# Kernel optimization log

Hardware: AMD Instinct MI355X
Metric: run time of the kernel (lower is better)

The kernel has to match this reference:

```python
import jax, jax.numpy as jnp
import numpy as np

B = 512; LH = 200; N = 40000; F = 256; E = 2000000; EF = 4
K = 8; LP = 50; P = 5000; D = 64; TD = 16; SK = 1000


def _time_enc(t):
    # TimeDualDecayEncoder stand-in: fixed log-spaced frequency cosine features (TGAT-style)
    freqs = 1.0 / (10.0 ** (jnp.arange(TD, dtype=jnp.float32) / TD * 5.0))
    return jnp.cos(t[..., None] * freqs)


def _layernorm(x, g, b):
    m = x.mean(-1, keepdims=True)
    v = ((x - m) ** 2).mean(-1, keepdims=True)
    return (x - m) * jax.lax.rsqrt(v + 1e-5) * g + b


def _gru(x, Wih, Whh, bih, bhh):
    # torch nn.GRU (batch_first), gate order r,z,n; returns final hidden state
    bsz, H = x.shape[0], Whh.shape[1]
    def step(h, xt):
        gi = xt @ Wih.T + bih
        gh = h @ Whh.T + bhh
        ir, iz, inn = jnp.split(gi, 3, -1)
        hr, hz, hn = jnp.split(gh, 3, -1)
        r = jax.nn.sigmoid(ir + hr)
        z = jax.nn.sigmoid(iz + hz)
        n = jnp.tanh(inn + r * hn)
        return (1.0 - z) * n + z * h, None
    h, _ = jax.lax.scan(step, jnp.zeros((bsz, H), x.dtype), jnp.swapaxes(x, 0, 1))
    return h


def _forward(src_node_ids, dst_node_ids, local_neighbor_ids, local_edge_ids, local_times,
             dst_neighbor_ids, dst_edge_ids, dst_times, retrieved_indices,
             node_raw, edge_raw, pool_nodes,
             Wfeat, bfeat, Wedge, bedge, Wtime, btime, Wstruct, bstruct, ln_g, ln_b,
             gruL_Wih, gruL_Whh, gruL_bih, gruL_bhh, gruQ_Wih, gruQ_Whh, gruQ_bih, gruQ_bhh,
             gcn_W, gcn_b, fus_W, fus_b, out_W, out_b):

    def dygkt(nids, eids, times, cur_dst, cur_skill):
        raw = node_raw[nids]                                   # (B,L,F) gather
        nf = raw @ Wfeat.T + bfeat
        ef = edge_raw[eids, 0:1] @ Wedge.T + bedge
        tf = _time_enc(times) @ Wtime.T + btime
        co = (nids == cur_dst[:, None]).astype(jnp.float32)[..., None]
        st = co @ Wstruct.T + bstruct
        sim = (raw[..., 0].astype(jnp.int32) == cur_skill[:, None]).astype(jnp.float32)[..., None]
        sk = sim @ Wstruct.T + bstruct
        return _layernorm(nf + ef + tf + st + sk, ln_g, ln_b)

    def graph_emb(demo):
        # demo: (K,LP) padded node-id sequences (0 = pad). Build dedup'd undirected
        # consecutive-pair graph, run GCNConv (self loops, sym norm), mean-pool.
        ids = demo.reshape(-1)
        M = ids.shape[0]
        valid = ids > 0
        sids = jnp.sort(jnp.where(valid, ids, N))               # invalid -> sentinel N
        uniq = (sids < N) & jnp.concatenate([jnp.ones((1,), bool), sids[1:] != sids[:-1]])
        x = node_raw[jnp.clip(sids, 0, N - 1)] @ Wfeat.T + bfeat
        h = (x @ gcn_W.T) * uniq[:, None]
        u = demo[:, :-1].reshape(-1)
        v = demo[:, 1:].reshape(-1)
        ve = (u > 0) & (v > 0)
        a = jnp.minimum(u, v); b = jnp.maximum(u, v)
        BIG = N * N                                             # fits int32 since N=40000
        skey = jnp.sort(jnp.where(ve, a * N + b, BIG))
        ew = ((skey < BIG) & jnp.concatenate([jnp.ones((1,), bool), skey[1:] != skey[:-1]])).astype(x.dtype)
        su = jnp.clip(jnp.searchsorted(sids, skey // N), 0, M - 1)
        sv = jnp.clip(jnp.searchsorted(sids, skey % N), 0, M - 1)
        uf = uniq.astype(x.dtype)
        deg = jnp.zeros(M, x.dtype).at[su].add(ew).at[sv].add(ew) + uf   # + self loop
        dis = jnp.where(deg > 0, jax.lax.rsqrt(deg), 0.0)
        nrm = (ew * dis[su] * dis[sv])[:, None]
        agg = jnp.zeros_like(h).at[sv].add(nrm * h[su]).at[su].add(nrm * h[sv])
        agg = agg + h * (dis * dis)[:, None] + gcn_b * uf[:, None]
        out = jax.nn.relu(agg)
        return out.sum(0) / jnp.maximum(uniq.sum(), 1).astype(x.dtype)

    dst_skill = node_raw[dst_node_ids, 0].astype(jnp.int32)
    src_skill = node_raw[src_node_ids, 0].astype(jnp.int32)
    local_emb = _gru(dygkt(local_neighbor_ids, local_edge_ids, local_times, dst_node_ids, dst_skill),
                     gruL_Wih, gruL_Whh, gruL_bih, gruL_bhh)
    glob = jax.vmap(graph_emb)(pool_nodes[retrieved_indices])   # (B,D)
    q_emb = _gru(dygkt(dst_neighbor_ids, dst_edge_ids, dst_times, src_node_ids, src_skill),
                 gruQ_Wih, gruQ_Whh, gruQ_bih, gruQ_bhh)
    fused = jax.nn.relu(jnp.concatenate([local_emb, glob], 1) @ fus_W.T + fus_b)
    return fused @ out_W.T + out_b, q_emb @ out_W.T + out_b


def setup_inputs() -> dict:
    key = jax.random.key(0)
    ks = jax.random.split(key, 32)
    f32 = jnp.float32
    node_raw = jax.random.normal(ks[0], (N, F), f32)
    node_raw = node_raw.at[:, 0].set(jax.random.randint(ks[1], (N,), 0, SK).astype(f32))
    edge_raw = jax.random.normal(ks[2], (E, EF), f32)
    ids = jax.random.randint(ks[3], (P, LP), 1, N)
    lens = jax.random.randint(ks[4], (P,), 2, LP + 1)
    pool_nodes = jnp.where(jnp.arange(LP)[None, :] < lens[:, None], ids, 0).astype(jnp.int32)
    def lin(k, o, i, s=0.05):
        kw, kb = jax.random.split(k)
        return jax.random.normal(kw, (o, i), f32) * s, jax.random.normal(kb, (o,), f32) * s
    Wfeat, bfeat = lin(ks[5], D, F)
    Wedge, bedge = lin(ks[6], D, 1)
    Wtime, btime = lin(ks[7], D, TD)
    Wstruct, bstruct = lin(ks[8], D, 1)
    gruL_Wih, gruL_bih = lin(ks[9], 3 * D, D)
    gruL_Whh, gruL_bhh = lin(ks[10], 3 * D, D)
    gruQ_Wih, gruQ_bih = lin(ks[11], 3 * D, D)
    gruQ_Whh, gruQ_bhh = lin(ks[12], 3 * D, D)
    gcn_W, gcn_b = lin(ks[13], D, D)
    fus_W, fus_b = lin(ks[14], D, 2 * D)
    out_W, out_b = lin(ks[15], D, D)
    return dict(
        src_node_ids=jax.random.randint(ks[16], (B,), 0, N).astype(jnp.int32),
        dst_node_ids=jax.random.randint(ks[17], (B,), 0, N).astype(jnp.int32),
        local_neighbor_ids=jax.random.randint(ks[18], (B, LH), 0, N).astype(jnp.int32),
        local_edge_ids=jax.random.randint(ks[19], (B, LH), 0, E).astype(jnp.int32),
        local_times=jax.random.uniform(ks[20], (B, LH), f32) * 100.0,
        dst_neighbor_ids=jax.random.randint(ks[21], (B, LH), 0, N).astype(jnp.int32),
        dst_edge_ids=jax.random.randint(ks[22], (B, LH), 0, E).astype(jnp.int32),
        dst_times=jax.random.uniform(ks[23], (B, LH), f32) * 100.0,
        retrieved_indices=jax.random.randint(ks[24], (B, K), 0, P).astype(jnp.int32),
        node_raw=node_raw, edge_raw=edge_raw, pool_nodes=pool_nodes,
        Wfeat=Wfeat, bfeat=bfeat, Wedge=Wedge, bedge=bedge, Wtime=Wtime, btime=btime,
        Wstruct=Wstruct, bstruct=bstruct, ln_g=jnp.ones((D,), f32), ln_b=jnp.zeros((D,), f32),
        gruL_Wih=gruL_Wih, gruL_Whh=gruL_Whh, gruL_bih=gruL_bih, gruL_bhh=gruL_bhh,
        gruQ_Wih=gruQ_Wih, gruQ_Whh=gruQ_Whh, gruQ_bih=gruQ_bih, gruQ_bhh=gruQ_bhh,
        gcn_W=gcn_W, gcn_b=gcn_b, fus_W=fus_W, fus_b=fus_b, out_W=out_W, out_b=out_b)


def reference(src_node_ids, dst_node_ids, local_neighbor_ids, local_edge_ids, local_times,
              dst_neighbor_ids, dst_edge_ids, dst_times, retrieved_indices,
              node_raw, edge_raw, pool_nodes,
              Wfeat, bfeat, Wedge, bedge, Wtime, btime, Wstruct, bstruct, ln_g, ln_b,
              gruL_Wih, gruL_Whh, gruL_bih, gruL_bhh, gruQ_Wih, gruQ_Whh, gruQ_bih, gruQ_bhh,
              gcn_W, gcn_b, fus_W, fus_b, out_W, out_b):
    return _forward(src_node_ids, dst_node_ids, local_neighbor_ids, local_edge_ids, local_times,
                    dst_neighbor_ids, dst_edge_ids, dst_times, retrieved_indices,
                    node_raw, edge_raw, pool_nodes,
                    Wfeat, bfeat, Wedge, bedge, Wtime, btime, Wstruct, bstruct, ln_g, ln_b,
                    gruL_Wih, gruL_Whh, gruL_bih, gruL_bhh, gruQ_Wih, gruQ_Whh, gruQ_bih, gruQ_bhh,
                    gcn_W, gcn_b, fus_W, fus_b, out_W, out_b)
```

## Files before the change

### kernel.cpp

```cpp
#include <hip/hip_runtime.h>
#include <math.h>

#define NN 40000
#define FF 256
#define DD 64
#define LHH 200
#define BB 512
#define TDD 16
#define GE_HASH 1024

typedef _Float16 h2f __attribute__((ext_vector_type(2)));

__constant__ float TFREQ[16] = {
    1.0f,            0.48696753f,    0.23713737f,    0.115478195f,
    0.056234132f,    0.027384196f,   0.013335215f,   0.0064938162f,
    0.0031622776f,   0.0015399265f,  0.00074989421f, 0.00036517414f,
    0.00017782794f,  8.6596433e-05f, 4.2169650e-05f, 2.0535251e-05f
};

__device__ __forceinline__ float fd2(unsigned a, unsigned b, float c) {
    union { unsigned u; h2f h; } ua, ub;
    ua.u = a; ub.u = b;
    return __builtin_amdgcn_fdot2(ua.h, ub.h, c, false);
}
__device__ __forceinline__ unsigned packrn(float a, float b) {
    union { h2f h; unsigned u; } x;
    x.h.x = (_Float16)a; x.h.y = (_Float16)b;
    return x.u;
}
__device__ __forceinline__ unsigned short f16u(float a) {
    union { _Float16 h; unsigned short u; } x;
    x.h = (_Float16)a;
    return x.u;
}
__device__ __forceinline__ float h16f(unsigned short u) {
    union { unsigned short u; _Float16 h; } x;
    x.u = u;
    return (float)x.h;
}
__device__ __forceinline__ float f16lo(unsigned u) {
    union { unsigned u; h2f h; } x; x.u = u; return (float)x.h.x;
}
__device__ __forceinline__ float f16hi(unsigned u) {
    union { unsigned u; h2f h; } x; x.u = u; return (float)x.h.y;
}
__device__ __forceinline__ unsigned pkrtz_u(float a, float b) {
    auto pk = __builtin_amdgcn_cvt_pkrtz(a, b);
    union { decltype(pk) h; unsigned u; } x;
    x.h = pk;
    return x.u;
}
__device__ __forceinline__ float dpp_xor1(float v) {
    return __int_as_float(
        __builtin_amdgcn_mov_dpp(__float_as_int(v), 0xB1, 0xF, 0xF, true));
}
__device__ __forceinline__ unsigned rlu(unsigned v, int l) {
    return (unsigned)__builtin_amdgcn_readlane((int)v, l);
}
__device__ __forceinline__ float sigm(float x) {
    return __builtin_amdgcn_rcpf(1.f + __expf(-x));
}
__device__ __forceinline__ float tanh_f(float x) {
    float e = __expf(2.f * x);
    return 1.f - 2.f * __builtin_amdgcn_rcpf(e + 1.f);
}
__device__ __forceinline__ int hlookupf(const unsigned* hkey, const int* hslot, unsigned id)
{
    unsigned p = (id * 2654435761u) & (GE_HASH - 1);
    while (hkey[p] != id) p = (p + 1) & (GE_HASH - 1);
    return hslot[p];
}

__global__ void __launch_bounds__(256)
compact_kernel(const float* __restrict__ node_raw, unsigned short* __restrict__ skill16)
{
    int i = blockIdx.x * 256 + threadIdx.x;
    if (i < NN) skill16[i] = (unsigned short)(int)node_raw[(size_t)i * FF];
}

template<int KDIM>
__global__ void __launch_bounds__(256)
gemm_nt_kernel(const float* __restrict__ A, const float* __restrict__ W,
               const float* __restrict__ bias, float* __restrict__ C, int Nrows)
{
    __shared__ __align__(16) float a_t[128][8];
    __shared__ __align__(16) float wt[8][64];
    const int tid = threadIdx.x;
    const int tx = tid & 15;
    const int ty = tid >> 4;
    const int n0 = blockIdx.x * 128;

    float4 acc[8];
#pragma unroll
    for (int r = 0; r < 8; ++r) acc[r] = make_float4(0.f, 0.f, 0.f, 0.f);

    for (int kc = 0; kc < KDIM; kc += 8) {
        __syncthreads();
        {
            int r = tid >> 1;
            int cc = (tid & 1) * 4;
            int n = n0 + r;
            float4 v = make_float4(0.f, 0.f, 0.f, 0.f);
            if (n < Nrows) v = *(const float4*)(A + (size_t)n * KDIM + kc + cc);
            *(float4*)&a_t[r][cc] = v;
        }
        {
            int m = tid >> 2;
            int f0 = (tid & 3) * 2;
            float2 v = *(const float2*)(W + (size_t)m * KDIM + kc + f0);
            wt[f0][m] = v.x; wt[f0 + 1][m] = v.y;
        }
        __syncthreads();
        float4 w4[8];
#pragma unroll
        for (int f = 0; f < 8; ++f) w4[f] = *(float4*)&wt[f][tx * 4];
#pragma unroll
        for (int rr = 0; rr < 8; ++rr) {
            int row = ty + rr * 16;
            float4 a0 = *(float4*)&a_t[row][0];
            float4 a1 = *(float4*)&a_t[row][4];
            float av[8] = {a0.x, a0.y, a0.z, a0.w, a1.x, a1.y, a1.z, a1.w};
#pragma unroll
            for (int f = 0; f < 8; ++f) {
                acc[rr].x += av[f] * w4[f].x;
                acc[rr].y += av[f] * w4[f].y;
                acc[rr].z += av[f] * w4[f].z;
                acc[rr].w += av[f] * w4[f].w;
            }
        }
    }
    float4 bv = make_float4(0.f, 0.f, 0.f, 0.f);
    if (bias) bv = *(const float4*)(bias + tx * 4);
#pragma unroll
    for (int rr = 0; rr < 8; ++rr) {
        int n = n0 + ty + rr * 16;
        if (n < Nrows) {
            float4 o = acc[rr];
            o.x += bv.x; o.y += bv.y; o.z += bv.z; o.w += bv.w;
            *(float4*)(C + (size_t)n * DD + tx * 4) = o;
        }
    }
}

__global__ void __launch_bounds__(256)
tn_gemm_kernel(const float* __restrict__ proj,
               const float* __restrict__ WihL, const float* __restrict__ WihQ,
               const float* __restrict__ ln_g,
               unsigned short* __restrict__ Tn4L, unsigned short* __restrict__ Tn4Q)
{
    const float* Wih = blockIdx.y ? WihQ : WihL;
    unsigned short* Tn4 = blockIdx.y ? Tn4Q : Tn4L;
    __shared__ float wgT[64][193];
    __shared__ __align__(16) float4 at4[64][16];
    const int tid = threadIdx.x;
    const int n0 = blockIdx.x * 64;
    for (int i = tid; i < 192 * 64; i += 256) {
        int j = i >> 6, k = i & 63;
        wgT[k][j] = Wih[i] * ln_g[k];
    }
    for (int i = tid; i < 1024; i += 256) {
        int r = i >> 4, kc = i & 15;
        at4[r][kc] = ((const float4*)(proj + (size_t)(n0 + r) * DD))[kc];
    }
    __syncthreads();
    const float* atf = (const float*)at4;
    const int c = tid & 63, wv = tid >> 6;
    float acc0[16], acc1[16], acc2[16];
#pragma unroll
    for (int r = 0; r < 16; ++r) { acc0[r] = 0.f; acc1[r] = 0.f; acc2[r] = 0.f; }
    for (int kc = 0; kc < 16; ++kc) {
        float w0[4], w1[4], w2[4];
#pragma unroll
        for (int q = 0; q < 4; ++q) {
            w0[q] = wgT[kc * 4 + q][c];
            w1[q] = wgT[kc * 4 + q][64 + c];
            w2[q] = wgT[kc * 4 + q][128 + c];
        }
#pragma unroll
        for (int r = 0; r < 16; ++r) {
            float4 a = at4[wv * 16 + r][kc];
            acc0[r] += a.x * w0[0] + a.y * w0[1] + a.z * w0[2] + a.w * w0[3];
            acc1[r] += a.x * w1[0] + a.y * w1[1] + a.z * w1[2] + a.w * w1[3];
            acc2[r] += a.x * w2[0] + a.y * w2[1] + a.z * w2[2] + a.w * w2[3];
        }
    }
#pragma unroll
    for (int r = 0; r < 16; ++r) {
        int row = wv * 16 + r;
        unsigned lo = packrn(acc0[r], acc1[r]);
        unsigned hi = packrn(acc2[r], atf[row * 64 + c]);
        uint2 o = make_uint2(lo, hi);
        *(uint2*)(Tn4 + ((size_t)(n0 + row) * 64 + c) * 4) = o;
    }
}

__global__ void __launch_bounds__(192)
consts_kernel(const float* __restrict__ WihL, const float* __restrict__ bihL,
              const float* __restrict__ WhhL, float* __restrict__ outL,
              unsigned* __restrict__ whpL, unsigned* __restrict__ tpkL,
              const float* __restrict__ WihQ, const float* __restrict__ bihQ,
              const float* __restrict__ WhhQ, float* __restrict__ outQ,
              unsigned* __restrict__ whpQ, unsigned* __restrict__ tpkQ,
              unsigned* __restrict__ wtpk,
              const float* __restrict__ ln_g, const float* __restrict__ ln_b,
              const float* __restrict__ Wedge, const float* __restrict__ bedge,
              const float* __restrict__ Wtime, const float* __restrict__ btime,
              const float* __restrict__ Wstruct, const float* __restrict__ bstruct)
{
    const float* Wih = blockIdx.x ? WihQ : WihL;
    const float* bih = blockIdx.x ? bihQ : bihL;
    const float* Whh = blockIdx.x ? WhhQ : WhhL;
    float* out = blockIdx.x ? outQ : outL;
    unsigned* whp = blockIdx.x ? whpQ : whpL;
    unsigned* tpk = blockIdx.x ? tpkQ : tpkL;
    const int j = threadIdx.x;
    float te = 0.f, tw = 0.f, t1 = 0.f, tb0 = 0.f, cc = 0.f;
    float tt[16];
#pragma unroll
    for (int t = 0; t < 16; ++t) tt[t] = 0.f;
    for (int k = 0; k < DD; ++k) {
        float wv = Wih[j * DD + k];
        float wg = wv * ln_g[k];
        te  += wg * Wedge[k];
        tw  += wg * Wstruct[k];
        t1  += wg;
        tb0 += wg * (bedge[k] + btime[k] + 2.f * bstruct[k]);
        cc  += wv * ln_b[k];
#pragma unroll
        for (int t = 0; t < 16; ++t) tt[t] += wg * Wtime[k * TDD + t];
    }
    out[0 * 192 + j] = te;
    out[1 * 192 + j] = tw;
    out[2 * 192 + j] = t1;
    out[3 * 192 + j] = tb0;
    out[4 * 192 + j] = cc + bih[j];
    for (int t = 0; t < 16; ++t) out[(5 + t) * 192 + j] = tt[t];
    for (int q = 0; q < 8; ++q)
        tpk[j * 8 + q] = packrn(tt[2 * q], tt[2 * q + 1]);
    if (blockIdx.x == 0 && j < 64)
        for (int q = 0; q < 8; ++q)
            wtpk[j * 8 + q] = packrn(Wtime[j * TDD + 2 * q], Wtime[j * TDD + 2 * q + 1]);
    for (int k2 = 0; k2 < 32; ++k2)
        whp[j * 32 + k2] = packrn(Whh[j * DD + 2 * k2], Whh[j * DD + 2 * k2 + 1]);
}

struct PS {
    int nid, skI;
    float tn0, tn1, tn2, pv, e0, t;
};

__global__ void __launch_bounds__(256)
pre_kernel(const int* __restrict__ nidsL, const int* __restrict__ eidsL,
           const float* __restrict__ timesL, const int* __restrict__ curL,
           const int* __restrict__ nidsQ, const int* __restrict__ eidsQ,
           const float* __restrict__ timesQ, const int* __restrict__ curQ,
           const unsigned short* __restrict__ skill16, const float* __restrict__ edge_raw,
           const unsigned short* __restrict__ Tn4L, const unsigned short* __restrict__ Tn4Q,
           const float* __restrict__ cstL, const float* __restrict__ cstQ,
           const unsigned* __restrict__ tpkL, const unsigned* __restrict__ tpkQ,
           const unsigned* __restrict__ wtpk,
           const float* __restrict__ bhhL, const float* __restrict__ bhhQ,
           const float* __restrict__ Wedge, const float* __restrict__ bedge,
           const float* __restrict__ Wtime, const float* __restrict__ btime,
           const float* __restrict__ Wstruct, const float* __restrict__ bstruct,
           unsigned* __restrict__ g01out, unsigned short* __restrict__ g2out)
{
    const int tid = threadIdx.x;
    const int d = tid & 63;
    const int seg = blockIdx.x * 4 + (tid >> 6);
    const int blk = seg >> 3, qq = seg & 7;
    const int g = blk >> 9, s = blk & 511;

    const int*            nids  = g ? nidsQ : nidsL;
    const int*            eids  = g ? eidsQ : eidsL;
    const float*          times = g ? timesQ : timesL;
    const int*            curp  = g ? curQ : curL;
    const unsigned short* Tn4   = g ? Tn4Q : Tn4L;
    const float*          cst   = g ? cstQ : cstL;
    const unsigned*       tpk   = g ? tpkQ : tpkL;
    const float*          bhh   = g ? bhhQ : bhhL;

    unsigned tp0[8], tp1[8], tp2[8], wtp[8];
#pragma unroll
    for (int q4 = 0; q4 < 2; ++q4) {
        uint4 a = *(const uint4*)(tpk + (size_t)(0 * 64 + d) * 8 + 4 * q4);
        tp0[4*q4] = a.x; tp0[4*q4+1] = a.y; tp0[4*q4+2] = a.z; tp0[4*q4+3] = a.w;
        uint4 b = *(const uint4*)(tpk + (size_t)(1 * 64 + d) * 8 + 4 * q4);
        tp1[4*q4] = b.x; tp1[4*q4+1] = b.y; tp1[4*q4+2] = b.z; tp1[4*q4+3] = b.w;
        uint4 c = *(const uint4*)(tpk + (size_t)(2 * 64 + d) * 8 + 4 * q4);
        tp2[4*q4] = c.x; tp2[4*q4+1] = c.y; tp2[4*q4+2] = c.z; tp2[4*q4+3] = c.w;
        uint4 e = *(const uint4*)(wtpk + (size_t)d * 8 + 4 * q4);
        wtp[4*q4] = e.x; wtp[4*q4+1] = e.y; wtp[4*q4+2] = e.z; wtp[4*q4+3] = e.w;
    }
    const float TE0 = cst[0*192 + d], TE1 = cst[0*192 + 64 + d], TE2 = cst[0*192 + 128 + d];
    const float TW0 = cst[1*192 + d], TW1 = cst[1*192 + 64 + d], TW2 = cst[1*192 + 128 + d];
    const float T10 = cst[2*192 + d], T11 = cst[2*192 + 64 + d], T12 = cst[2*192 + 128 + d];
    const float TB0 = cst[3*192 + d], TB1 = cst[3*192 + 64 + d], TB2 = cst[3*192 + 128 + d];
    const float CC0 = cst[4*192 + d] + bhh[d];
    const float CC1 = cst[4*192 + 64 + d] + bhh[64 + d];
    const float CC2 = cst[4*192 + 128 + d];
    const float we_l = Wedge[d];
    const float ws_l = Wstruct[d];
    const float b0_l = bedge[d] + btime[d] + 2.f * bstruct[d];
    const float tfl  = TFREQ[d & 15];

    const int cur = curp[s];
    const int csk = (int)skill16[cur];
    const int* nrow = nids + s * LHH;
    const int* erow = eids + s * LHH;
    const float* trow = times + s * LHH;
    const int lbase = qq * 25;

    auto GATH = [&](PS& P, int i) {
        int l = lbase + i;
        int nid = nrow[l];
        int eid = erow[l];
        P.nid = nid;
        uint2 v = *(const uint2*)(Tn4 + ((size_t)nid * 64 + d) * 4);
        P.tn0 = f16lo(v.x);
        P.tn1 = f16hi(v.x);
        P.tn2 = f16lo(v.y);
        P.pv  = f16hi(v.y);
        P.e0  = edge_raw[(size_t)eid * 4];
        P.skI = (int)skill16[nid];
        P.t   = trow[l];
    };

    auto EMIT = [&](const PS& P, int i) {
        float cv = __cosf(P.t * tfl);
        float cx = dpp_xor1(cv);
        unsigned cp = pkrtz_u(cv, cx);
        unsigned s0 = rlu(cp, 0),  s1 = rlu(cp, 2),  s2 = rlu(cp, 4),  s3 = rlu(cp, 6);
        unsigned s4 = rlu(cp, 8),  s5 = rlu(cp, 10), s6 = rlu(cp, 12), s7 = rlu(cp, 14);
        float tf = fd2(wtp[7], s7, fd2(wtp[6], s6, fd2(wtp[5], s5, fd2(wtp[4], s4, 0.f))));
        tf = fd2(wtp[3], s3, fd2(wtp[2], s2, fd2(wtp[1], s1, fd2(wtp[0], s0, tf))));
        float flg = ((P.nid == cur) ? 1.f : 0.f) + ((P.skI == csk) ? 1.f : 0.f);
        float f = P.pv + P.e0 * we_l + flg * ws_l + b0_l + tf;
        float mu = f;
#pragma unroll
        for (int off = 32; off; off >>= 1) mu += __shfl_xor(mu, off);
        mu *= (1.f / 64.f);
        float dv = f - mu, var = dv * dv;
#pragma unroll
        for (int off = 32; off; off >>= 1) var += __shfl_xor(var, off);
        float rs = rsqrtf(var * (1.f / 64.f) + 1e-5f);
        float c0 = fd2(tp0[7], s7, fd2(tp0[6], s6, fd2(tp0[5], s5, fd2(tp0[4], s4, 0.f))));
        c0 = fd2(tp0[3], s3, fd2(tp0[2], s2, fd2(tp0[1], s1, fd2(tp0[0], s0, c0))));
        float c1 = fd2(tp1[7], s7, fd2(tp1[6], s6, fd2(tp1[5], s5, fd2(tp1[4], s4, 0.f))));
        c1 = fd2(tp1[3], s3, fd2(tp1[2], s2, fd2(tp1[1], s1, fd2(tp1[0], s0, c1))));
        float c2 = fd2(tp2[7], s7, fd2(tp2[6], s6, fd2(tp2[5], s5, fd2(tp2[4], s4, 0.f))));
        c2 = fd2(tp2[3], s3, fd2(tp2[2], s2, fd2(tp2[1], s1, fd2(tp2[0], s0, c2))));
        float g0 = (c0 + P.tn0 + P.e0 * TE0 + flg * TW0 + TB0 - mu * T10) * rs + CC0;
        float g1 = (c1 + P.tn1 + P.e0 * TE1 + flg * TW1 + TB1 - mu * T11) * rs + CC1;
        float g2 = (c2 + P.tn2 + P.e0 * TE2 + flg * TW2 + TB2 - mu * T12) * rs + CC2;
        size_t pos = ((size_t)blk * LHH + (lbase + i)) * 64 + d;
        g01out[pos] = packrn(g0, g1);
        g2out[pos] = f16u(g2);
    };

    PS A, B, C;
    GATH(A, 0);
    GATH(B, 1);
    for (int i = 0; i < 25; ++i) {
        int inext = (i + 2 < 25) ? i + 2 : 24;
        GATH(C, inext);
        EMIT(A, i);
        A = B; B = C;
    }
}

__global__ void __launch_bounds__(64) __attribute__((amdgpu_waves_per_eu(1, 1)))
gru_lite_kernel(const unsigned* __restrict__ g01, const unsigned short* __restrict__ g2a,
                const unsigned* __restrict__ whpL, const unsigned* __restrict__ whpQ,
                const float* __restrict__ bhhL, const float* __restrict__ bhhQ,
                float* __restrict__ embL, float* __restrict__ embQ)
{
    const int blk = blockIdx.x;
    const int g = blk >> 9, s = blk & 511;
    const int d = threadIdx.x;

    const unsigned* whp = g ? whpQ : whpL;
    const float*    bhh = g ? bhhQ : bhhL;
    float*          emb = g ? embQ : embL;

    unsigned w0[32], w1[32], w2[32];
    {
        const unsigned* p0 = whp + (size_t)d * 32;
        const unsigned* p1 = whp + (size_t)(64 + d) * 32;
        const unsigned* p2 = whp + (size_t)(128 + d) * 32;
#pragma unroll
        for (int q4 = 0; q4 < 8; ++q4) {
            uint4 a = *(const uint4*)(p0 + 4 * q4);
            w0[4*q4] = a.x; w0[4*q4+1] = a.y; w0[4*q4+2] = a.z; w0[4*q4+3] = a.w;
            uint4 b = *(const uint4*)(p1 + 4 * q4);
            w1[4*q4] = b.x; w1[4*q4+1] = b.y; w1[4*q4+2] = b.z; w1[4*q4+3] = b.w;
            uint4 c = *(const uint4*)(p2 + 4 * q4);
            w2[4*q4] = c.x; w2[4*q4+1] = c.y; w2[4*q4+2] = c.z; w2[4*q4+3] = c.w;
        }
    }
#pragma unroll
    for (int i = 0; i < 32; ++i) {
        asm volatile("" : "+v"(w0[i]));
        asm volatile("" : "+v"(w1[i]));
        asm volatile("" : "+v"(w2[i]));
    }
    const float BH2 = bhh[128 + d];

    const unsigned* p01 = g01 + (size_t)blk * LHH * 64 + d;
    const unsigned short* p2 = g2a + (size_t)blk * LHH * 64 + d;

    float h = 0.f;

    auto COMPUTE = [&](unsigned pk01, unsigned pk2) {
        float g0 = f16lo(pk01), g1 = f16hi(pk01);
        float g2 = h16f((unsigned short)pk2);
        float hx = dpp_xor1(h);
        unsigned hpu = pkrtz_u(h, hx);
        float a0 = 0.f, a1 = 0.f, a2 = 0.f, e0 = 0.f, e1 = 0.f, e2 = 0.f;
#pragma unroll
        for (int q = 0; q < 32; q += 2) {
            unsigned sa = rlu(hpu, 2 * q);
            unsigned sb = rlu(hpu, 2 * q + 2);
            a0 = fd2(w0[q], sa, a0);
            a1 = fd2(w1[q], sa, a1);
            a2 = fd2(w2[q], sa, a2);
            e0 = fd2(w0[q+1], sb, e0);
            e1 = fd2(w1[q+1], sb, e1);
            e2 = fd2(w2[q+1], sb, e2);
        }
        float mv0 = a0 + e0, mv1 = a1 + e1, mv2 = a2 + e2;
        float r = sigm(g0 + mv0);
        float z = sigm(g1 + mv1);
        float n = tanh_f(g2 + r * (mv2 + BH2));
        h = (1.f - z) * n + z * h;
    };

    unsigned A01[4], A2[4], B01[4], B2[4];
#pragma unroll
    for (int i = 0; i < 4; ++i) {
        A01[i] = p01[(size_t)i * 64];
        A2[i]  = p2[(size_t)i * 64];
    }
    for (int l = 0; l < LHH; l += 8) {
#pragma unroll
        for (int i = 0; i < 4; ++i) {
            int ll = l + 4 + i;
            B01[i] = p01[(size_t)ll * 64];
            B2[i]  = p2[(size_t)ll * 64];
        }
#pragma unroll
        for (int i = 0; i < 4; ++i) COMPUTE(A01[i], A2[i]);
#pragma unroll
        for (int i = 0; i < 4; ++i) {
            int ll = l + 8 + i;
            if (ll > LHH - 1) ll = LHH - 1;
            A01[i] = p01[(size_t)ll * 64];
            A2[i]  = p2[(size_t)ll * 64];
        }
#pragma unroll
        for (int i = 0; i < 4; ++i) COMPUTE(B01[i], B2[i]);
    }
    emb[(size_t)s * DD + d] = h;
}

__global__ void __launch_bounds__(512)
dedup_kernel(const int* __restrict__ retrieved, const int* __restrict__ pool_nodes,
             int* __restrict__ slot_idG, float* __restrict__ disG,
             unsigned* __restrict__ startG, unsigned short* __restrict__ adjG,
             int* __restrict__ Ub)
{
    __shared__ unsigned hkey[GE_HASH];
    __shared__ int hslot[GE_HASH];
    __shared__ unsigned ekey[GE_HASH];
    __shared__ int ids[400];
    __shared__ int slot_id[400];
    __shared__ unsigned deg[400];
    __shared__ float dis[400];
    __shared__ unsigned elist[400];
    __shared__ unsigned scanA[400], scanB[400];
    __shared__ int cursor[400];
    __shared__ unsigned short adjS[800];
    __shared__ int pids[8];
    __shared__ int cntU, cntE;

    const int b = blockIdx.x;
    const int tid = threadIdx.x;

    if (tid < 8) pids[tid] = retrieved[b * 8 + tid];
    if (tid == 0) { cntU = 0; cntE = 0; }
    for (int i = tid; i < GE_HASH; i += 512) { hkey[i] = 0u; ekey[i] = 0u; }
    if (tid < 400) deg[tid] = 0u;
    __syncthreads();

    if (tid < 400) {
        int k = tid / 50, p = tid % 50;
        ids[tid] = pool_nodes[(size_t)pids[k] * 50 + p];
    }
    __syncthreads();

    if (tid < 400) {
        int idi = ids[tid];
        if (idi > 0) {
            unsigned id = (unsigned)idi;
            unsigned p = (id * 2654435761u) & (GE_HASH - 1);
            while (true) {
                unsigned old = atomicCAS(&hkey[p], 0u, id);
                if (old == 0u) {
                    int s = atomicAdd(&cntU, 1);
                    hslot[p] = s; slot_id[s] = idi;
                    break;
                }
                if (old == id) break;
                p = (p + 1) & (GE_HASH - 1);
            }
        }
    }
    __syncthreads();

    if (tid < 8 * 49) {
        int k = tid / 49, p = tid % 49;
        int u = ids[k * 50 + p], v = ids[k * 50 + p + 1];
        if (u > 0 && v > 0) {
            unsigned a = (unsigned)min(u, v), bb = (unsigned)max(u, v);
            unsigned key = a * 40000u + bb;
            unsigned p2 = (key * 2654435761u) & (GE_HASH - 1);
            while (true) {
                unsigned old = atomicCAS(&ekey[p2], 0u, key);
                if (old == 0u) {
                    int su = hlookupf(hkey, hslot, a);
                    int sv = hlookupf(hkey, hslot, bb);
                    int e = atomicAdd(&cntE, 1);
                    elist[e] = ((unsigned)su << 16) | (unsigned)sv;
                    atomicAdd(&deg[su], 1u);
                    atomicAdd(&deg[sv], 1u);
                    break;
                }
                if (old == key) break;
                p2 = (p2 + 1) & (GE_HASH - 1);
            }
        }
    }
    __syncthreads();

    const int U = cntU, EC = cntE;
    if (tid < 400) {
        dis[tid] = rsqrtf((float)deg[tid] + 1.0f);
        scanA[tid] = deg[tid];
    }
    __syncthreads();

    unsigned* src = scanA;
    unsigned* dst = scanB;
    for (int off = 1; off < 400; off <<= 1) {
        if (tid < 400)
            dst[tid] = src[tid] + ((tid >= off) ? src[tid - off] : 0u);
        __syncthreads();
        unsigned* t = src; src = dst; dst = t;
    }
    if (tid < 400) {
        unsigned st = src[tid] - deg[tid];
        cursor[tid] = (int)st;
        if (tid < U) startG[(size_t)b * 404 + tid] = st;
    }
    if (tid == 0) {
        startG[(size_t)b * 404 + U] = (U > 0) ? src[U - 1] : 0u;
        Ub[b] = U;
    }
    __syncthreads();

    if (tid < EC) {
        unsigned pk = elist[tid];
        int su = (int)(pk >> 16), sv = (int)(pk & 0xffffu);
        int pu = atomicAdd(&cursor[su], 1);
        adjS[pu] = (unsigned short)sv;
        int pv = atomicAdd(&cursor[sv], 1);
        adjS[pv] = (unsigned short)su;
    }
    __syncthreads();

    if (tid < 400) {
        slot_idG[(size_t)b * 400 + tid] = (tid < U) ? slot_id[tid] : 0;
        disG[(size_t)b * 400 + tid] = dis[tid];
    }
    for (int i = tid; i < 800; i += 512) {
        unsigned tot = (U > 0) ? src[U - 1] : 0u;
        adjG[(size_t)b * 800 + i] = (i < (int)tot) ? adjS[i] : (unsigned short)0;
    }
}

__global__ void __launch_bounds__(256)
gcn_agg_kernel(const float* __restrict__ hgcn, const float* __restrict__ gcn_b,
               const int* __restrict__ slot_idG, const float* __restrict__ disG,
               const unsigned* __restrict__ startG, const unsigned short* __restrict__ adjG,
               const int* __restrict__ Ub, float* __restrict__ part)
{
    __shared__ int sidS[400];
    __shared__ float disS[400];
    __shared__ unsigned stS[404];
    __shared__ unsigned short adjS[800];
    __shared__ float red[4][64];

    const int b = blockIdx.x, q = blockIdx.y;
    const int tid = threadIdx.x;
    const int lane = tid & 63, w = tid >> 6;
    const int U = Ub[b];

    for (int i = tid; i < 400; i += 256) {
        sidS[i] = slot_idG[(size_t)b * 400 + i];
        disS[i] = disG[(size_t)b * 400 + i];
    }
    for (int i = tid; i < 404; i += 256) stS[i] = startG[(size_t)b * 404 + i];
    for (int i = tid; i < 800; i += 256) adjS[i] = adjG[(size_t)b * 800 + i];
    __syncthreads();

    const float gb = gcn_b[lane];
    float acc = 0.f;

    for (int s = q * 4 + w; s < U; s += 16) {
        int nid = sidS[s];
        float ds = disS[s];
        float v = fmaf(ds * ds, hgcn[(size_t)nid * 64 + lane], gb);
        int a0 = (int)stS[s];
        int cnt = (int)stS[s + 1] - a0;
        for (int e0 = 0; e0 < cnt; e0 += 4) {
            float hv[4], nr[4];
#pragma unroll
            for (int j = 0; j < 4; ++j) {
                int e = e0 + j;
                int ec = (e < cnt) ? e : cnt - 1;
                int o = adjS[a0 + ec];
                nr[j] = (e < cnt) ? ds * disS[o] : 0.f;
                hv[j] = hgcn[(size_t)sidS[o] * 64 + lane];
            }
            v += nr[0] * hv[0] + nr[1] * hv[1] + nr[2] * hv[2] + nr[3] * hv[3];
        }
        acc += fmaxf(v, 0.f);
    }

    red[w][lane] = acc;
    __syncthreads();
    if (tid < 64)
        part[((size_t)b * 4 + q) * 64 + tid] =
            red[0][tid] + red[1][tid] + red[2][tid] + red[3][tid];
}

__global__ void __launch_bounds__(64)
head_kernel(const float* __restrict__ local_emb, const float* __restrict__ part,
            const int* __restrict__ Ub, const float* __restrict__ q_emb,
            const float* __restrict__ fus_W, const float* __restrict__ fus_b,
            const float* __restrict__ out_W, const float* __restrict__ out_b,
            float* __restrict__ out)
{
    __shared__ float cat[128];
    __shared__ float fus[64];
    __shared__ float qv[64];
    const int b = blockIdx.x, d = threadIdx.x;
    cat[d] = local_emb[(size_t)b * 64 + d];
    {
        const float* pb = part + (size_t)b * 4 * 64;
        float gsum = pb[d] + pb[64 + d] + pb[128 + d] + pb[192 + d];
        cat[64 + d] = gsum / (float)max(Ub[b], 1);
    }
    qv[d] = q_emb[(size_t)b * 64 + d];
    __syncthreads();
    float acc = fus_b[d];
    const float* fw = fus_W + (size_t)d * 128;
#pragma unroll 4
    for (int k = 0; k < 128; ++k) acc += cat[k] * fw[k];
    fus[d] = fmaxf(acc, 0.f);
    __syncthreads();
    float o0 = out_b[d], o1 = out_b[d];
    const float* ow = out_W + (size_t)d * 64;
#pragma unroll 4
    for (int k = 0; k < 64; ++k) { float ww = ow[k]; o0 += fus[k] * ww; o1 += qv[k] * ww; }
    out[(size_t)b * 64 + d] = o0;
    out[(size_t)BB * 64 + (size_t)b * 64 + d] = o1;
}

extern "C" void kernel_launch(void* const* d_in, const int* in_sizes, int n_in,
                              void* d_out, int out_size, void* d_ws, size_t ws_size,
                              hipStream_t stream)
{
    const int*   src_ids    = (const int*)d_in[0];
    const int*   dst_ids    = (const int*)d_in[1];
    const int*   l_nids     = (const int*)d_in[2];
    const int*   l_eids     = (const int*)d_in[3];
    const float* l_times    = (const float*)d_in[4];
    const int*   d_nids     = (const int*)d_in[5];
    const int*   d_eids     = (const int*)d_in[6];
    const float* d_times    = (const float*)d_in[7];
    const int*   retr       = (const int*)d_in[8];
    const float* node_raw   = (const float*)d_in[9];
    const float* edge_raw   = (const float*)d_in[10];
    const int*   pool_nodes = (const int*)d_in[11];
    const float* Wfeat  = (const float*)d_in[12];
    const float* bfeat  = (const float*)d_in[13];
    const float* Wedge  = (const float*)d_in[14];
    const float* bedge  = (const float*)d_in[15];
    const float* Wtime  = (const float*)d_in[16];
    const float* btime  = (const float*)d_in[17];
    const float* Wstruct= (const float*)d_in[18];
    const float* bstruct= (const float*)d_in[19];
    const float* ln_g   = (const float*)d_in[20];
    const float* ln_b   = (const float*)d_in[21];
    const float* gruL_Wih = (const float*)d_in[22];
    const float* gruL_Whh = (const float*)d_in[23];
    const float* gruL_bih = (const float*)d_in[24];
    const float* gruL_bhh = (const float*)d_in[25];
    const float* gruQ_Wih = (const float*)d_in[26];
    const float* gruQ_Whh = (const float*)d_in[27];
    const float* gruQ_bih = (const float*)d_in[28];
    const float* gruQ_bhh = (const float*)d_in[29];
    const float* gcn_W  = (const float*)d_in[30];
    const float* gcn_b  = (const float*)d_in[31];
    const float* fus_W  = (const float*)d_in[32];
    const float* fus_b  = (const float*)d_in[33];
    const float* out_W  = (const float*)d_in[34];
    const float* out_b  = (const float*)d_in[35];

    char* wsb = (char*)d_ws;
    auto alloc = [&](size_t bytes) -> void* {
        void* p = (void*)wsb;
        wsb += (bytes + 255) & ~(size_t)255;
        return p;
    };
    float*          proj_node = (float*)alloc((size_t)NN * DD * 4);
    float*          hgcn      = (float*)alloc((size_t)NN * DD * 4);
    unsigned short* Tn4L      = (unsigned short*)alloc((size_t)NN * 64 * 4 * 2);
    unsigned short* Tn4Q      = (unsigned short*)alloc((size_t)NN * 64 * 4 * 2);
    unsigned short* skill16   = (unsigned short*)alloc((size_t)NN * 2);
    float*          cstL      = (float*)alloc(4096 * 4);
    float*          cstQ      = (float*)alloc(4096 * 4);
    unsigned*       whpL      = (unsigned*)alloc(192 * 32 * 4);
    unsigned*       whpQ      = (unsigned*)alloc(192 * 32 * 4);
    unsigned*       tpkL      = (unsigned*)alloc(192 * 8 * 4);
    unsigned*       tpkQ      = (unsigned*)alloc(192 * 8 * 4);
    unsigned*       wtpk      = (unsigned*)alloc(64 * 8 * 4);
    unsigned*       g01       = (unsigned*)alloc((size_t)2 * BB * LHH * 64 * 4);
    unsigned short* g2a       = (unsigned short*)alloc((size_t)2 * BB * LHH * 64 * 2);
    int*            slot_idG  = (int*)alloc((size_t)BB * 400 * 4);
    float*          disG      = (float*)alloc((size_t)BB * 400 * 4);
    unsigned*       startG    = (unsigned*)alloc((size_t)BB * 404 * 4);
    unsigned short* adjG      = (unsigned short*)alloc((size_t)BB * 800 * 2);
    int*            Ubuf      = (int*)alloc((size_t)BB * 4);
    float*          part      = (float*)alloc((size_t)BB * 4 * 64 * 4);
    float*          local_emb = (float*)alloc((size_t)BB * DD * 4);
    float*          q_emb     = (float*)alloc((size_t)BB * DD * 4);

    dim3 g1((NN + 127) / 128);
    gemm_nt_kernel<FF><<<g1, 256, 0, stream>>>(node_raw, Wfeat, bfeat, proj_node, NN);

    compact_kernel<<<(NN + 255) / 256, 256, 0, stream>>>(node_raw, skill16);

    consts_kernel<<<2, 192, 0, stream>>>(gruL_Wih, gruL_bih, gruL_Whh, cstL, whpL, tpkL,
                                         gruQ_Wih, gruQ_bih, gruQ_Whh, cstQ, whpQ, tpkQ,
                                         wtpk, ln_g, ln_b, Wedge, bedge, Wtime, btime,
                                         Wstruct, bstruct);

    gemm_nt_kernel<DD><<<g1, 256, 0, stream>>>(proj_node, gcn_W, nullptr, hgcn, NN);

    tn_gemm_kernel<<<dim3(NN / 64, 2), 256, 0, stream>>>(proj_node, gruL_Wih, gruQ_Wih,
                                                         ln_g, Tn4L, Tn4Q);

    dedup_kernel<<<BB, 512, 0, stream>>>(retr, pool_nodes, slot_idG, disG,
                                         startG, adjG, Ubuf);

    pre_kernel<<<2 * BB * 2, 256, 0, stream>>>(
        l_nids, l_eids, l_times, dst_ids,
        d_nids, d_eids, d_times, src_ids,
        skill16, edge_raw, Tn4L, Tn4Q, cstL, cstQ,
        tpkL, tpkQ, wtpk, gruL_bhh, gruQ_bhh,
        Wedge, bedge, Wtime, btime, Wstruct, bstruct,
        g01, g2a);

    gcn_agg_kernel<<<dim3(BB, 4), 256, 0, stream>>>(
        hgcn, gcn_b, slot_idG, disG, startG, adjG, Ubuf, part);

    gru_lite_kernel<<<2 * BB, 64, 0, stream>>>(
        g01, g2a, whpL, whpQ, gruL_bhh, gruQ_bhh, local_emb, q_emb);

    head_kernel<<<BB, 64, 0, stream>>>(local_emb, part, Ubuf, q_emb,
        fus_W, fus_b, out_W, out_b, (float*)d_out);
}
```

Measured before the change: 292.9 us.

## Precompute LayerNorm mean algebraically to remove one wave reduction per row

The LayerNorm mean in pre_kernel is now computed analytically from precomputed per-node row sums of the projected features plus summed weight constants, so only the variance needs a cross-lane reduction. compact_kernel now also writes each node's projected-feature sum packed with its skill id into an 8-byte record, and consts_kernel emits the weight-sum constants. The remaining variance reduction uses DPP row operations instead of a full shuffle chain. This adds a pass over proj_node and slightly larger per-neighbor gathers, and the time-encoding part of the mean is computed with fp16 dot products, which may shift rounding.

Result: no change. 295.2 us (+0.8%).

```diff
diff --git a/kernel.cpp b/kernel.cpp
--- a/kernel.cpp
+++ b/kernel.cpp
@@ -54,6 +54,21 @@
     return __int_as_float(
         __builtin_amdgcn_mov_dpp(__float_as_int(v), 0xB1, 0xF, 0xF, true));
 }
+template<int CTRL>
+__device__ __forceinline__ float dppadd(float v) {
+    float t = __int_as_float(
+        __builtin_amdgcn_mov_dpp(__float_as_int(v), CTRL, 0xF, 0xF, true));
+    return v + t;
+}
+__device__ __forceinline__ float wave_sum64(float v) {
+    v = dppadd<0xB1>(v);
+    v = dppadd<0x4E>(v);
+    v = dppadd<0x141>(v);
+    v = dppadd<0x140>(v);
+    v += __shfl_xor(v, 16);
+    v += __shfl_xor(v, 32);
+    return v;
+}
 __device__ __forceinline__ unsigned rlu(unsigned v, int l) {
     return (unsigned)__builtin_amdgcn_readlane((int)v, l);
 }
@@ -72,10 +87,18 @@
 }
 
 __global__ void __launch_bounds__(256)
-compact_kernel(const float* __restrict__ node_raw, unsigned short* __restrict__ skill16)
-{
-    int i = blockIdx.x * 256 + threadIdx.x;
-    if (i < NN) skill16[i] = (unsigned short)(int)node_raw[(size_t)i * FF];
+compact_kernel(const float* __restrict__ node_raw, const float* __restrict__ proj,
+               uint2* __restrict__ node8)
+{
+    const int n = blockIdx.x * 4 + (threadIdx.x >> 6);
+    const int d = threadIdx.x & 63;
+    if (n >= NN) return;
+    float v = proj[(size_t)n * DD + d];
+    v = wave_sum64(v);
+    if (d == 0) {
+        unsigned sk = (unsigned)(int)node_raw[(size_t)n * FF];
+        node8[n] = make_uint2(sk, __float_as_uint(v));
+    }
 }
 
 template<int KDIM>
@@ -201,7 +224,7 @@
               const float* __restrict__ WihQ, const float* __restrict__ bihQ,
               const float* __restrict__ WhhQ, float* __restrict__ outQ,
               unsigned* __restrict__ whpQ, unsigned* __restrict__ tpkQ,
-              unsigned* __restrict__ wtpk,
+              unsigned* __restrict__ wtpk, float* __restrict__ mcst,
               const float* __restrict__ ln_g, const float* __restrict__ ln_b,
               const float* __restrict__ Wedge, const float* __restrict__ bedge,
               const float* __restrict__ Wtime, const float* __restrict__ btime,
@@ -240,13 +263,33 @@
     if (blockIdx.x == 0 && j < 64)
         for (int q = 0; q < 8; ++q)
             wtpk[j * 8 + q] = packrn(Wtime[j * TDD + 2 * q], Wtime[j * TDD + 2 * q + 1]);
+    if (blockIdx.x == 0 && j < 16) {
+        float s = 0.f;
+        for (int k = 0; k < DD; ++k) s += Wtime[k * TDD + j];
+        mcst[j] = s;
+    }
+    if (blockIdx.x == 0 && j == 16) {
+        float s = 0.f;
+        for (int k = 0; k < DD; ++k) s += Wedge[k];
+        mcst[16] = s;
+    }
+    if (blockIdx.x == 0 && j == 17) {
+        float s = 0.f;
+        for (int k = 0; k < DD; ++k) s += Wstruct[k];
+        mcst[17] = s;
+    }
+    if (blockIdx.x == 0 && j == 18) {
+        float s = 0.f;
+        for (int k = 0; k < DD; ++k) s += bedge[k] + btime[k] + 2.f * bstruct[k];
+        mcst[18] = s;
+    }
     for (int k2 = 0; k2 < 32; ++k2)
         whp[j * 32 + k2] = packrn(Whh[j * DD + 2 * k2], Whh[j * DD + 2 * k2 + 1]);
 }
 
 struct PS {
     int nid, skI;
-    float tn0, tn1, tn2, pv, e0, t;
+    float tn0, tn1, tn2, pv, e0, t, spv;
 };
 
 __global__ void __launch_bounds__(256)
@@ -254,11 +297,11 @@
            const float* __restrict__ timesL, const int* __restrict__ curL,
            const int* __restrict__ nidsQ, const int* __restrict__ eidsQ,
            const float* __restrict__ timesQ, const int* __restrict__ curQ,
-           const unsigned short* __restrict__ skill16, const float* __restrict__ edge_raw,
+           const uint2* __restrict__ node8, const float* __restrict__ edge_raw,
            const unsigned short* __restrict__ Tn4L, const unsigned short* __restrict__ Tn4Q,
            const float* __restrict__ cstL, const float* __restrict__ cstQ,
            const unsigned* __restrict__ tpkL, const unsigned* __restrict__ tpkQ,
-           const unsigned* __restrict__ wtpk,
+           const unsigned* __restrict__ wtpk, const float* __restrict__ mcst,
            const float* __restrict__ bhhL, const float* __restrict__ bhhQ,
            const float* __restrict__ Wedge, const float* __restrict__ bedge,
            const float* __restrict__ Wtime, const float* __restrict__ btime,
@@ -280,7 +323,7 @@
     const unsigned*       tpk   = g ? tpkQ : tpkL;
     const float*          bhh   = g ? bhhQ : bhhL;
 
-    unsigned tp0[8], tp1[8], tp2[8], wtp[8];
+    unsigned tp0[8], tp1[8], tp2[8], wtp[8], csp[8];
 #pragma unroll
     for (int q4 = 0; q4 < 2; ++q4) {
         uint4 a = *(const uint4*)(tpk + (size_t)(0 * 64 + d) * 8 + 4 * q4);
@@ -292,6 +335,11 @@
         uint4 e = *(const uint4*)(wtpk + (size_t)d * 8 + 4 * q4);
         wtp[4*q4] = e.x; wtp[4*q4+1] = e.y; wtp[4*q4+2] = e.z; wtp[4*q4+3] = e.w;
     }
+#pragma unroll
+    for (int q = 0; q < 8; ++q)
+        csp[q] = packrn(mcst[2 * q], mcst[2 * q + 1]);
+    const float SWe = mcst[16], SWs = mcst[17], Sb0 = mcst[18];
+
     const float TE0 = cst[0*192 + d], TE1 = cst[0*192 + 64 + d], TE2 = cst[0*192 + 128 + d];
     const float TW0 = cst[1*192 + d], TW1 = cst[1*192 + 64 + d], TW2 = cst[1*192 + 128 + d];
     const float T10 = cst[2*192 + d], T11 = cst[2*192 + 64 + d], T12 = cst[2*192 + 128 + d];
@@ -305,7 +353,7 @@
     const float tfl  = TFREQ[d & 15];
 
     const int cur = curp[s];
-    const int csk = (int)skill16[cur];
+    const int csk = (int)node8[cur].x;
     const int* nrow = nids + s * LHH;
     const int* erow = eids + s * LHH;
     const float* trow = times + s * LHH;
@@ -322,7 +370,9 @@
         P.tn2 = f16lo(v.y);
         P.pv  = f16hi(v.y);
         P.e0  = edge_raw[(size_t)eid * 4];
-        P.skI = (int)skill16[nid];
+        uint2 nr = node8[nid];
+        P.skI = (int)nr.x;
+        P.spv = __uint_as_float(nr.y);
         P.t   = trow[l];
     };
 
@@ -335,15 +385,13 @@
         float tf = fd2(wtp[7], s7, fd2(wtp[6], s6, fd2(wtp[5], s5, fd2(wtp[4], s4, 0.f))));
         tf = fd2(wtp[3], s3, fd2(wtp[2], s2, fd2(wtp[1], s1, fd2(wtp[0], s0, tf))));
         float flg = ((P.nid == cur) ? 1.f : 0.f) + ((P.skI == csk) ? 1.f : 0.f);
+        float stf = fd2(csp[7], s7, fd2(csp[6], s6, fd2(csp[5], s5, fd2(csp[4], s4, 0.f))));
+        stf = fd2(csp[3], s3, fd2(csp[2], s2, fd2(csp[1], s1, fd2(csp[0], s0, stf))));
+        float mu = (P.spv + P.e0 * SWe + flg * SWs + Sb0 + stf) * (1.f / 64.f);
         float f = P.pv + P.e0 * we_l + flg * ws_l + b0_l + tf;
-        float mu = f;
-#pragma unroll
-        for (int off = 32; off; off >>= 1) mu += __shfl_xor(mu, off);
-        mu *= (1.f / 64.f);
-        float dv = f - mu, var = dv * dv;
-#pragma unroll
-        for (int off = 32; off; off >>= 1) var += __shfl_xor(var, off);
-        float rs = rsqrtf(var * (1.f / 64.f) + 1e-5f);
+        float dv = f - mu;
+        float var = wave_sum64(dv * dv) * (1.f / 64.f);
+        float rs = rsqrtf(var + 1e-5f);
         float c0 = fd2(tp0[7], s7, fd2(tp0[6], s6, fd2(tp0[5], s5, fd2(tp0[4], s4, 0.f))));
         c0 = fd2(tp0[3], s3, fd2(tp0[2], s2, fd2(tp0[1], s1, fd2(tp0[0], s0, c0))));
         float c1 = fd2(tp1[7], s7, fd2(tp1[6], s6, fd2(tp1[5], s5, fd2(tp1[4], s4, 0.f))));
@@ -728,7 +776,7 @@
     float*          hgcn      = (float*)alloc((size_t)NN * DD * 4);
     unsigned short* Tn4L      = (unsigned short*)alloc((size_t)NN * 64 * 4 * 2);
     unsigned short* Tn4Q      = (unsigned short*)alloc((size_t)NN * 64 * 4 * 2);
-    unsigned short* skill16   = (unsigned short*)alloc((size_t)NN * 2);
+    uint2*          node8     = (uint2*)alloc((size_t)NN * 8);
     float*          cstL      = (float*)alloc(4096 * 4);
     float*          cstQ      = (float*)alloc(4096 * 4);
     unsigned*       whpL      = (unsigned*)alloc(192 * 32 * 4);
@@ -736,6 +784,7 @@
     unsigned*       tpkL      = (unsigned*)alloc(192 * 8 * 4);
     unsigned*       tpkQ      = (unsigned*)alloc(192 * 8 * 4);
     unsigned*       wtpk      = (unsigned*)alloc(64 * 8 * 4);
+    float*          mcst      = (float*)alloc(32 * 4);
     unsigned*       g01       = (unsigned*)alloc((size_t)2 * BB * LHH * 64 * 4);
     unsigned short* g2a       = (unsigned short*)alloc((size_t)2 * BB * LHH * 64 * 2);
     int*            slot_idG  = (int*)alloc((size_t)BB * 400 * 4);
@@ -750,11 +799,11 @@
     dim3 g1((NN + 127) / 128);
     gemm_nt_kernel<FF><<<g1, 256, 0, stream>>>(node_raw, Wfeat, bfeat, proj_node, NN);
 
-    compact_kernel<<<(NN + 255) / 256, 256, 0, stream>>>(node_raw, skill16);
+    compact_kernel<<<NN / 4, 256, 0, stream>>>(node_raw, proj_node, node8);
 
     consts_kernel<<<2, 192, 0, stream>>>(gruL_Wih, gruL_bih, gruL_Whh, cstL, whpL, tpkL,
                                          gruQ_Wih, gruQ_bih, gruQ_Whh, cstQ, whpQ, tpkQ,
-                                         wtpk, ln_g, ln_b, Wedge, bedge, Wtime, btime,
+                                         wtpk, mcst, ln_g, ln_b, Wedge, bedge, Wtime, btime,
                                          Wstruct, bstruct);
 
     gemm_nt_kernel<DD><<<g1, 256, 0, stream>>>(proj_node, gcn_W, nullptr, hgcn, NN);
@@ -768,8 +817,8 @@
     pre_kernel<<<2 * BB * 2, 256, 0, stream>>>(
         l_nids, l_eids, l_times, dst_ids,
         d_nids, d_eids, d_times, src_ids,
-        skill16, edge_raw, Tn4L, Tn4Q, cstL, cstQ,
-        tpkL, tpkQ, wtpk, gruL_bhh, gruQ_bhh,
+        node8, edge_raw, Tn4L, Tn4Q, cstL, cstQ,
+        tpkL, tpkQ, wtpk, mcst, gruL_bhh, gruQ_bhh,
         Wedge, bedge, Wtime, btime, Wstruct, bstruct,
         g01, g2a);
 
```
